# Optimization experiments

Measured on AMD Instinct MI355X. Metric: run time of the kernel, lower is better.

Reference implementation:

```python
import jax, jax.numpy as jnp
import numpy as np

B, N, C, H = 4, 1024, 1024, 16
D = C // H  # head_dim = 64
SCALE = D ** -0.5


def setup_inputs() -> dict:
    key = jax.random.key(0)
    ks = jax.random.split(key, 7)
    std = 0.02
    return {
        "xq": jax.random.normal(ks[0], (B, N, C), dtype=jnp.float32),
        "xk": jax.random.normal(ks[1], (B, N, C), dtype=jnp.float32),
        "xv": jax.random.normal(ks[2], (B, N, C), dtype=jnp.float32),
        # torch nn.Linear weights are [out_features, in_features]
        "Wq": jax.random.normal(ks[3], (C, C), dtype=jnp.float32) * std,
        "Wkv": jax.random.normal(ks[4], (2 * C, C), dtype=jnp.float32) * std,
        "Wp": jax.random.normal(ks[5], (C, C), dtype=jnp.float32) * std,
        "bp": jax.random.normal(ks[6], (C,), dtype=jnp.float32) * std,
    }


def reference(xq, xk, xv, Wq, Wkv, Wp, bp):
    b, nq, c = xq.shape
    nk = xk.shape[1]
    # q projection -> [B, H, Nq, D]
    q = (xq @ Wq.T).reshape(b, nq, H, D).transpose(0, 2, 1, 3)
    # HPA: shared projection produces K and V from xk (xv unused)
    kv = xk @ Wkv.T  # [B, Nk, 2C]
    k, v = jnp.split(kv, 2, axis=-1)
    k = k.reshape(b, nk, H, D).transpose(0, 2, 1, 3)  # [B, H, Nk, D]
    v = v.reshape(b, nk, H, D).transpose(0, 2, 1, 3)  # [B, H, Nk, D]
    # pre-softmax scores (attn_save in original)
    attn = jnp.einsum("bhqd,bhkd->bhqk", q, k) * SCALE  # [B, H, Nq, Nk]
    p = jax.nn.softmax(attn, axis=-1)
    x = jnp.einsum("bhqk,bhkd->bhqd", p, v)  # [B, H, Nq, D]
    x = x.transpose(0, 2, 1, 3).reshape(b, nq, c)
    x = x @ Wp.T + bp
    # returns (x transposed to [Nq, B, C], mean-over-heads pre-softmax scores)
    return x.transpose(1, 0, 2), attn.sum(axis=1) / H
```

## Files before the change

kernel.cpp:

```cpp
#include <hip/hip_runtime.h>
#include <hip/hip_bf16.h>
#include <stdint.h>

typedef __attribute__((ext_vector_type(8))) short bf16x8;
typedef __attribute__((ext_vector_type(4))) short bf16x4;
typedef __attribute__((ext_vector_type(4))) float f32x4;

#define B_DIM 4
#define N_DIM 1024
#define C_DIM 1024
#define NT 16

#define QSCALE 0.18033688011112042f
#define OUT1_ALPHA 0.04332169878499658f

__device__ __forceinline__ ushort f2bf(float f) {
  union { float f; uint32_t u; } v; v.f = f;
  uint32_t r = (v.u + 0x7FFFu + ((v.u >> 16) & 1u)) >> 16;
  return (ushort)r;
}

__device__ __forceinline__ uint32_t cvtpk(float lo, float hi) {
  uint32_t r;
  asm("v_cvt_pk_bf16_f32 %0, %1, %2" : "=v"(r) : "v"(lo), "v"(hi));
  return r;
}

__device__ __forceinline__ void gload_lds16(const void* g, void* l) {
  __builtin_amdgcn_global_load_lds(
      (const __attribute__((address_space(1))) void*)g,
      (__attribute__((address_space(3))) void*)l, 16, 0, 0);
}

__device__ __forceinline__ f32x4 mfma16(bf16x8 a, bf16x8 b, f32x4 c) {
  return __builtin_amdgcn_mfma_f32_16x16x32_bf16(a, b, c, 0, 0, 0);
}

__device__ __forceinline__ void mfma16x16(bf16x4 a, bf16x4 b, f32x4& c) {
  asm("v_mfma_f32_16x16x16_bf16 %0, %1, %2, %0" : "+v"(c) : "v"(a), "v"(b));
}

template <int N>
__device__ __forceinline__ void waitcnt_vm() {
  asm volatile("s_waitcnt vmcnt(%0)" ::"i"(N) : "memory");
}

__global__ __launch_bounds__(256) void cvt_all(
    const float* __restrict__ xq, const float* __restrict__ xk,
    const float* __restrict__ Wq, const float* __restrict__ Wkv,
    const float* __restrict__ Wp, ushort* __restrict__ xq_b,
    ushort* __restrict__ xk_b, ushort* __restrict__ Wq_b,
    ushort* __restrict__ Wkv_b, ushort* __restrict__ Wp_b) {
  int bid = blockIdx.x;
  const float* s;
  ushort* d;
  int off;
  if (bid < 4096) { s = xq; d = xq_b; off = bid; }
  else if (bid < 8192) { s = xk; d = xk_b; off = bid - 4096; }
  else if (bid < 9216) { s = Wq; d = Wq_b; off = bid - 8192; }
  else if (bid < 11264) { s = Wkv; d = Wkv_b; off = bid - 9216; }
  else { s = Wp; d = Wp_b; off = bid - 11264; }
  int i = off * 1024 + threadIdx.x * 4;
  float4 v = *(const float4*)(s + i);
  ushort4 o;
  o.x = f2bf(v.x); o.y = f2bf(v.y); o.z = f2bf(v.z); o.w = f2bf(v.w);
  *(ushort4*)(d + i) = o;
}

template <int MODE, int BN>
__device__ __forceinline__ void gemm_core(
    ushort* As, ushort* Bs, const ushort* A, const ushort* Bm, float* Cf,
    ushort* Cb, int K, int lda, int ldb, int ldc, int m0, int n0, float alpha,
    const float* bias) {
  constexpr int MR = (BN == 128) ? 4 : 2;
  constexpr int WM = (BN == 128) ? 64 : 32;
  constexpr int ABUF = 4096, BBUF = BN * 32;
  constexpr int NLD = (BN == 128) ? 4 : 3;
  const int tid = threadIdx.x;
  const int l = tid & 63, wv = tid >> 6, lg = l >> 4, lr = l & 15;
  const int wr = (BN == 128) ? (wv >> 1) : wv;
  const int wc = (BN == 128) ? (wv & 1) : 0;
  const int r0 = tid >> 2;
  const int cs = ((tid & 3) ^ ((r0 >> 1) & 3)) * 8;
  const int wb = (tid & ~63) * 8;
  const int cA = ((lg ^ ((lr >> 1) & 3)) << 3);
  const ushort* Ar0 = A + (size_t)(m0 + r0) * lda + cs;
  const ushort* Ar1 = A + (size_t)(m0 + 64 + r0) * lda + cs;
  const ushort* Br0 = Bm + (size_t)(n0 + r0) * ldb + cs;
  const ushort* Br1 = Bm + (size_t)(n0 + 64 + r0) * ldb + cs;

#define STAGE(t, bi)                                                     \
  {                                                                      \
    const int k0_ = (t) << 5;                                            \
    gload_lds16(Ar0 + k0_, As + (bi) * ABUF + wb);                       \
    gload_lds16(Ar1 + k0_, As + (bi) * ABUF + 2048 + wb);                \
    gload_lds16(Br0 + k0_, Bs + (bi) * BBUF + wb);                       \
    if (BN == 128) gload_lds16(Br1 + k0_, Bs + (bi) * BBUF + 2048 + wb); \
  }

  const int nk = K >> 5;
  STAGE(0, 0);
  STAGE(1, 1);
  f32x4 acc[MR][4] = {};
  waitcnt_vm<NLD>();
  __builtin_amdgcn_sched_barrier(0);
  __builtin_amdgcn_s_barrier();
  __builtin_amdgcn_sched_barrier(0);
  int b0 = 0;
  for (int t = 0; t < nk; ++t) {
    const int b2 = (b0 + 2 >= 3) ? b0 - 1 : b0 + 2;
    if (t + 2 < nk) STAGE(t + 2, b2);
    const ushort* Ab = As + b0 * ABUF;
    const ushort* Bb = Bs + b0 * BBUF;
    bf16x8 af[MR], bfr[4];
#pragma unroll
    for (int m = 0; m < MR; m++)
      af[m] = *(const bf16x8*)&Ab[(wr * WM + m * 16 + lr) * 32 + cA];
#pragma unroll
    for (int n = 0; n < 4; n++)
      bfr[n] = *(const bf16x8*)&Bb[(wc * 64 + n * 16 + lr) * 32 + cA];
    __builtin_amdgcn_s_setprio(1);
#pragma unroll
    for (int m = 0; m < MR; m++)
#pragma unroll
      for (int n = 0; n < 4; n++)
        acc[m][n] = mfma16(af[m], bfr[n], acc[m][n]);
    __builtin_amdgcn_s_setprio(0);
    if (t + 1 < nk) {
      if (t + 2 < nk) waitcnt_vm<NLD>(); else waitcnt_vm<0>();
      __builtin_amdgcn_sched_barrier(0);
      __builtin_amdgcn_s_barrier();
      __builtin_amdgcn_sched_barrier(0);
    }
    b0 = (b0 + 1 >= 3) ? 0 : b0 + 1;
  }
#undef STAGE

#pragma unroll
  for (int m = 0; m < MR; m++) {
    const int row = m0 + wr * WM + m * 16 + lg * 4;
#pragma unroll
    for (int n = 0; n < 4; n++) {
      const int col = n0 + wc * 64 + n * 16 + lr;
#pragma unroll
      for (int r = 0; r < 4; r++) {
        float v = acc[m][n][r];
        if (MODE == 0) {
          Cb[(size_t)(row + r) * ldc + col] = f2bf(v * alpha);
        } else if (MODE == 1) {
          Cf[(size_t)(row + r) * ldc + col] = v * alpha;
        } else {
          int gm = row + r;
          int bb = gm >> 10, nq = gm & 1023;
          Cf[((size_t)nq * B_DIM + bb) * C_DIM + col] = v + bias[col];
        }
      }
    }
  }
}

template <int MODE, int BN>
__global__ __launch_bounds__(256) void gemm_bt(
    const ushort* __restrict__ A, const ushort* __restrict__ Bm,
    float* __restrict__ Cf, ushort* __restrict__ Cb, int K, int lda, int ldb,
    int ldc, long sA, long sB, long sC, float alpha,
    const float* __restrict__ bias) {
  __shared__ ushort As[3 * 4096];
  __shared__ ushort Bs[3 * BN * 32];
  const int z = blockIdx.z;
  float* cf = (MODE == 0) ? nullptr : (Cf + (size_t)z * sC);
  ushort* cb = (MODE == 0) ? (Cb + (size_t)z * sC) : nullptr;
  gemm_core<MODE, BN>(As, Bs, A + (size_t)z * sA, Bm + (size_t)z * sB, cf, cb,
                      K, lda, ldb, ldc, blockIdx.y * 128, blockIdx.x * BN,
                      alpha, bias);
}

__global__ __launch_bounds__(256) void gemm_dual(
    const ushort* __restrict__ A0, const ushort* __restrict__ B0,
    ushort* __restrict__ C0, const ushort* __restrict__ A1,
    const ushort* __restrict__ B1, ushort* __restrict__ C1) {
  __shared__ ushort As[3 * 4096];
  __shared__ ushort Bs[3 * 4096];
  int bid = blockIdx.x;
  if (bid < 256) {
    gemm_core<0, 128>(As, Bs, A0, B0, nullptr, C0, 1024, 1024, 1024, 1024,
                      (bid >> 3) * 128, (bid & 7) * 128, QSCALE, nullptr);
  } else {
    bid -= 256;
    gemm_core<0, 128>(As, Bs, A1, B1, nullptr, C1, 1024, 1024, 1024, 2048,
                      (bid >> 4) * 128, (bid & 15) * 128, 1.f, nullptr);
  }
}

__global__ __launch_bounds__(256) void flash_out1(
    const ushort* __restrict__ Qp, const ushort* __restrict__ KVp,
    ushort* __restrict__ O, float* __restrict__ out1) {
  __shared__ ushort sm[20480];
  int bid = blockIdx.x;

  if (bid >= 1024) {
    int b2 = bid - 1024;
    int z = b2 >> 7;
    gemm_core<1, 64>(sm, sm + 12288, Qp + (size_t)z * 1048576,
                     KVp + (size_t)z * 2097152, out1 + (size_t)z * 1048576,
                     nullptr, 1024, 1024, 2048, 1024, ((b2 >> 4) & 7) * 128,
                     (b2 & 15) * 64, OUT1_ALPHA, nullptr);
    return;
  }

  ushort* Ks0 = sm;
  ushort* Vs0 = sm + 8192;
  ushort* Qs = sm + 16384;

  const int tid = threadIdx.x;
  const int w = tid >> 6, l = tid & 63;
  const int lg = l >> 4, lr = l & 15;
  const int bh = bid >> 4;
  const int b = bh >> 4, h = bh & 15;
  const int q0 = (bid & 15) * 64;

  const ushort* Qg =
      Qp + (size_t)b * (N_DIM * C_DIM) + (size_t)q0 * C_DIM + h * 64;
  const ushort* Kg = KVp + (size_t)b * (N_DIM * 2 * C_DIM) + h * 64;
  const ushort* Vg = Kg + C_DIM;

  const int sr = tid >> 3;
  const int sc = (tid & 7) ^ (sr & 7);
  const int wb = (tid & ~63) * 8;
  const int vrow = (l & 31) >> 1;
  const int vdc = ((l >> 5) << 4) + (l & 1) * 8;

#define STAGE_K(kt2, buf)                                                   \
  {                                                                         \
    gload_lds16(Kg + (size_t)((kt2) + sr) * 2048 + sc * 8, (buf) + wb);     \
    gload_lds16(Kg + (size_t)((kt2) + 32 + sr) * 2048 + sc * 8,             \
                (buf) + 2048 + wb);                                         \
  }
#define STAGE_V(kt2, buf)                                                   \
  {                                                                         \
    gload_lds16(Vg + (size_t)((kt2) + w * 16 + vrow) * 2048 + vdc,          \
                (buf) + (w * 4 + 0) * 256);                                 \
    gload_lds16(Vg + (size_t)((kt2) + w * 16 + vrow) * 2048 + 32 + vdc,     \
                (buf) + (w * 4 + 2) * 256);                                 \
  }

  gload_lds16(Qg + (size_t)sr * C_DIM + sc * 8, Qs + wb);
  gload_lds16(Qg + (size_t)(32 + sr) * C_DIM + sc * 8, Qs + 2048 + wb);
  STAGE_K(0, Ks0);
  STAGE_V(0, Vs0);
  __syncthreads();
  const int qrow = w * 16 + lr;
  bf16x8 qa0 = *(const bf16x8*)&Qs[qrow * 64 + ((lg ^ (qrow & 7)) << 3)];
  bf16x8 qa1 = *(const bf16x8*)&Qs[qrow * 64 + (((lg + 4) ^ (qrow & 7)) << 3)];

  f32x4 oacc[4] = {};
  float lp = 0.f;
  const uint32_t vbase =
      (uint32_t)(uintptr_t)(__attribute__((address_space(3))) ushort*)Vs0 +
      (uint32_t)(l * 8);

  for (int t = 0; t < NT; ++t) {
    const int cur = t & 1;
    ushort* Kc = Ks0 + cur * 4096;
    if (t + 1 < NT) {
      const int kt2 = (t + 1) * 64;
      STAGE_K(kt2, Ks0 + (cur ^ 1) * 4096);
      STAGE_V(kt2, Vs0 + (cur ^ 1) * 4096);
    }

    f32x4 s[4];
    __builtin_amdgcn_s_setprio(1);
#pragma unroll
    for (int kf = 0; kf < 4; kf++) {
      const int krow = kf * 16 + lr;
      bf16x8 kb0 = *(const bf16x8*)&Kc[krow * 64 + ((lg ^ (krow & 7)) << 3)];
      bf16x8 kb1 =
          *(const bf16x8*)&Kc[krow * 64 + (((lg + 4) ^ (krow & 7)) << 3)];
      f32x4 zz = {};
      zz = mfma16(kb0, qa0, zz);
      zz = mfma16(kb1, qa1, zz);
      s[kf] = zz;
    }
    __builtin_amdgcn_s_setprio(0);

    bf16x4 pa[4];
#pragma unroll
    for (int kf = 0; kf < 4; kf++) {
      float p0 = exp2f(s[kf][0]), p1 = exp2f(s[kf][1]);
      float p2 = exp2f(s[kf][2]), p3 = exp2f(s[kf][3]);
      lp += (p0 + p1) + (p2 + p3);
      union { uint32_t u[2]; bf16x4 v; } pk;
      pk.u[0] = cvtpk(p0, p1);
      pk.u[1] = cvtpk(p2, p3);
      pa[kf] = pk.v;
    }

    const uint32_t trb = vbase + cur * 8192;
    __builtin_amdgcn_s_setprio(1);
#define PV_DF(df, O0, O1, O2, O3)                                          \
  {                                                                        \
    bf16x4 v0, v1, v2, v3;                                                 \
    asm volatile("ds_read_b64_tr_b16 %0, %1 offset:" #O0                   \
                 : "=v"(v0) : "v"(trb));                                   \
    asm volatile("ds_read_b64_tr_b16 %0, %1 offset:" #O1                   \
                 : "=v"(v1) : "v"(trb));                                   \
    asm volatile("ds_read_b64_tr_b16 %0, %1 offset:" #O2                   \
                 : "=v"(v2) : "v"(trb));                                   \
    asm volatile("ds_read_b64_tr_b16 %0, %1 offset:" #O3                   \
                 : "=v"(v3) : "v"(trb));                                   \
    asm volatile("s_waitcnt lgkmcnt(0)" ::: "memory");                     \
    __builtin_amdgcn_sched_barrier(0);                                     \
    mfma16x16(pa[0], v0, oacc[df]);                                        \
    mfma16x16(pa[1], v1, oacc[df]);                                        \
    mfma16x16(pa[2], v2, oacc[df]);                                        \
    mfma16x16(pa[3], v3, oacc[df]);                                        \
  }
    PV_DF(0, 0, 2048, 4096, 6144)
    PV_DF(1, 512, 2560, 4608, 6656)
    PV_DF(2, 1024, 3072, 5120, 7168)
    PV_DF(3, 1536, 3584, 5632, 7680)
#undef PV_DF
    __builtin_amdgcn_s_setprio(0);

    __syncthreads();
  }
#undef STAGE_K
#undef STAGE_V

  lp += __shfl_xor(lp, 16);
  lp += __shfl_xor(lp, 32);
  float linv[4];
#pragma unroll
  for (int r = 0; r < 4; r++) linv[r] = 1.0f / __shfl(lp, lg * 4 + r);

  ushort* Og = O + (size_t)b * (N_DIM * C_DIM) +
               (size_t)(q0 + w * 16 + lg * 4) * C_DIM + h * 64;
#pragma unroll
  for (int df = 0; df < 4; df++)
#pragma unroll
    for (int r = 0; r < 4; r++)
      Og[(size_t)r * C_DIM + df * 16 + lr] = f2bf(oacc[df][r] * linv[r]);
}

extern "C" void kernel_launch(void* const* d_in, const int* in_sizes, int n_in,
                              void* d_out, int out_size, void* d_ws,
                              size_t ws_size, hipStream_t stream) {
  const float* xq = (const float*)d_in[0];
  const float* xk = (const float*)d_in[1];
  const float* Wq = (const float*)d_in[3];
  const float* Wkv = (const float*)d_in[4];
  const float* Wp = (const float*)d_in[5];
  const float* bp = (const float*)d_in[6];

  ushort* ws = (ushort*)d_ws;
  ushort* xq_b = ws;
  ushort* xk_b = xq_b + 4194304;
  ushort* Wq_b = xk_b + 4194304;
  ushort* Wkv_b = Wq_b + 1048576;
  ushort* Wp_b = Wkv_b + 2097152;
  ushort* Qp = Wp_b + 1048576;
  ushort* KVp = Qp + 4194304;
  ushort* Ob = KVp + 8388608;

  float* out0 = (float*)d_out;
  float* out1 = out0 + 4194304;

  cvt_all<<<12288, 256, 0, stream>>>(xq, xk, Wq, Wkv, Wp, xq_b, xk_b, Wq_b,
                                     Wkv_b, Wp_b);
  gemm_dual<<<768, 256, 0, stream>>>(xq_b, Wq_b, Qp, xk_b, Wkv_b, KVp);
  flash_out1<<<1536, 256, 0, stream>>>(Qp, KVp, Ob, out1);
  gemm_bt<2, 64><<<dim3(16, 32, 1), 256, 0, stream>>>(
      Ob, Wp_b, out0, nullptr, 1024, 1024, 1024, 1024, 0, 0, 0, 1.f, bp);
}
```

Baseline: 213.8 us.

## Replace 256-thread GEMMs with single-wave 64x64 tile GEMM kernels

Swaps the 4-wave 128x128 (and 128x64) tiled GEMMs for Q/KV projection and the output projection with a new single-wave kernel. Each block computes a 64x64 tile, loads directly into LDS and double-buffers it with a 2-stage prefetch. This gives many more, smaller blocks and avoids cross-wave synchronisation. In exchange each tile reuses less data, so global/L2 traffic per FLOP goes up.

```diff
diff --git a/kernel.cpp b/kernel.cpp
--- a/kernel.cpp
+++ b/kernel.cpp
@@ -65,6 +65,109 @@
   ushort4 o;
   o.x = f2bf(v.x); o.y = f2bf(v.y); o.z = f2bf(v.z); o.w = f2bf(v.w);
   *(ushort4*)(d + i) = o;
+}
+
+template <int MODE>
+__device__ __forceinline__ void gemm_nb_core(
+    ushort* Ls, const ushort* A, const ushort* Bm, int lda, int ldb,
+    float* Cf, ushort* Cb, int ldc, int crow0, int ccol0, float alpha,
+    const float* bias) {
+  const int l = threadIdx.x & 63;
+  const int lg = l >> 4, lr = l & 15;
+  const int cs = ((l & 3) ^ ((l >> 3) & 3)) * 8;
+  const ushort* Ar = A + (size_t)(l >> 2) * lda + cs;
+  const ushort* Br = Bm + (size_t)(l >> 2) * ldb + cs;
+  ushort* LA = Ls;
+  ushort* LB = Ls + 4096;
+  const int cA = (lg ^ ((lr >> 1) & 3)) << 3;
+
+#define NBSTAGE(t, bi)                                          \
+  {                                                             \
+    const int k0_ = (t) << 5;                                   \
+    gload_lds16(Ar + k0_, LA + (bi) * 2048);                    \
+    gload_lds16(Ar + (size_t)16 * lda + k0_, LA + (bi) * 2048 + 512);  \
+    gload_lds16(Ar + (size_t)32 * lda + k0_, LA + (bi) * 2048 + 1024); \
+    gload_lds16(Ar + (size_t)48 * lda + k0_, LA + (bi) * 2048 + 1536); \
+    gload_lds16(Br + k0_, LB + (bi) * 2048);                    \
+    gload_lds16(Br + (size_t)16 * ldb + k0_, LB + (bi) * 2048 + 512);  \
+    gload_lds16(Br + (size_t)32 * ldb + k0_, LB + (bi) * 2048 + 1024); \
+    gload_lds16(Br + (size_t)48 * ldb + k0_, LB + (bi) * 2048 + 1536); \
+  }
+
+  f32x4 acc[4][4] = {};
+  NBSTAGE(0, 0);
+  NBSTAGE(1, 1);
+  for (int t = 0; t < 32; ++t) {
+    if (t + 1 < 32) waitcnt_vm<8>(); else waitcnt_vm<0>();
+    const int bo = (t & 1) * 2048;
+    bf16x8 af[4], bf[4];
+#pragma unroll
+    for (int m = 0; m < 4; m++)
+      af[m] = *(const bf16x8*)&LA[bo + (m * 16 + lr) * 32 + cA];
+#pragma unroll
+    for (int n = 0; n < 4; n++)
+      bf[n] = *(const bf16x8*)&LB[bo + (n * 16 + lr) * 32 + cA];
+    __builtin_amdgcn_s_setprio(1);
+#pragma unroll
+    for (int m = 0; m < 4; m++)
+#pragma unroll
+      for (int n = 0; n < 4; n++)
+        acc[m][n] = mfma16(af[m], bf[n], acc[m][n]);
+    __builtin_amdgcn_s_setprio(0);
+    if (t + 2 < 32) NBSTAGE(t + 2, t & 1);
+  }
+#undef NBSTAGE
+
+#pragma unroll
+  for (int m = 0; m < 4; m++) {
+    const int row = crow0 + m * 16 + lg * 4;
+#pragma unroll
+    for (int n = 0; n < 4; n++) {
+      const int col = ccol0 + n * 16 + lr;
+#pragma unroll
+      for (int r = 0; r < 4; r++) {
+        float v = acc[m][n][r];
+        if (MODE == 0) {
+          Cb[(size_t)(row + r) * ldc + col] = f2bf(v * alpha);
+        } else {
+          int gm = row + r;
+          int bb = gm >> 10, nq = gm & 1023;
+          Cf[((size_t)nq * B_DIM + bb) * C_DIM + col] = v + bias[col];
+        }
+      }
+    }
+  }
+}
+
+__global__ __launch_bounds__(64) void gemm_nb_dual(
+    const ushort* __restrict__ xq_b, const ushort* __restrict__ xk_b,
+    const ushort* __restrict__ Wq_b, const ushort* __restrict__ Wkv_b,
+    ushort* __restrict__ Qp, ushort* __restrict__ KVp) {
+  __shared__ ushort Ls[8192];
+  int bid = blockIdx.x;
+  if (bid < 1024) {
+    int mt = bid >> 4, nt = bid & 15;
+    gemm_nb_core<0>(Ls, xq_b + (size_t)mt * 64 * 1024,
+                    Wq_b + (size_t)nt * 64 * 1024, 1024, 1024, nullptr, Qp,
+                    1024, mt * 64, nt * 64, QSCALE, nullptr);
+  } else {
+    int b2 = bid - 1024;
+    int mt = b2 >> 5, nt = b2 & 31;
+    gemm_nb_core<0>(Ls, xk_b + (size_t)mt * 64 * 1024,
+                    Wkv_b + (size_t)nt * 64 * 1024, 1024, 1024, nullptr, KVp,
+                    2048, mt * 64, nt * 64, 1.f, nullptr);
+  }
+}
+
+__global__ __launch_bounds__(64) void gemm_nb_proj(
+    const ushort* __restrict__ Ob, const ushort* __restrict__ Wp_b,
+    float* __restrict__ out0, const float* __restrict__ bias) {
+  __shared__ ushort Ls[8192];
+  int bid = blockIdx.x;
+  int mt = bid >> 4, nt = bid & 15;
+  gemm_nb_core<2>(Ls, Ob + (size_t)mt * 64 * 1024,
+                  Wp_b + (size_t)nt * 64 * 1024, 1024, 1024, out0, nullptr,
+                  1024, mt * 64, nt * 64, 1.f, bias);
 }
 
 template <int MODE, int BN>
@@ -159,39 +262,6 @@
   }
 }
 
-template <int MODE, int BN>
-__global__ __launch_bounds__(256) void gemm_bt(
-    const ushort* __restrict__ A, const ushort* __restrict__ Bm,
-    float* __restrict__ Cf, ushort* __restrict__ Cb, int K, int lda, int ldb,
-    int ldc, long sA, long sB, long sC, float alpha,
-    const float* __restrict__ bias) {
-  __shared__ ushort As[3 * 4096];
-  __shared__ ushort Bs[3 * BN * 32];
-  const int z = blockIdx.z;
-  float* cf = (MODE == 0) ? nullptr : (Cf + (size_t)z * sC);
-  ushort* cb = (MODE == 0) ? (Cb + (size_t)z * sC) : nullptr;
-  gemm_core<MODE, BN>(As, Bs, A + (size_t)z * sA, Bm + (size_t)z * sB, cf, cb,
-                      K, lda, ldb, ldc, blockIdx.y * 128, blockIdx.x * BN,
-                      alpha, bias);
-}
-
-__global__ __launch_bounds__(256) void gemm_dual(
-    const ushort* __restrict__ A0, const ushort* __restrict__ B0,
-    ushort* __restrict__ C0, const ushort* __restrict__ A1,
-    const ushort* __restrict__ B1, ushort* __restrict__ C1) {
-  __shared__ ushort As[3 * 4096];
-  __shared__ ushort Bs[3 * 4096];
-  int bid = blockIdx.x;
-  if (bid < 256) {
-    gemm_core<0, 128>(As, Bs, A0, B0, nullptr, C0, 1024, 1024, 1024, 1024,
-                      (bid >> 3) * 128, (bid & 7) * 128, QSCALE, nullptr);
-  } else {
-    bid -= 256;
-    gemm_core<0, 128>(As, Bs, A1, B1, nullptr, C1, 1024, 1024, 1024, 2048,
-                      (bid >> 4) * 128, (bid & 15) * 128, 1.f, nullptr);
-  }
-}
-
 __global__ __launch_bounds__(256) void flash_out1(
     const ushort* __restrict__ Qp, const ushort* __restrict__ KVp,
     ushort* __restrict__ O, float* __restrict__ out1) {
@@ -367,8 +437,7 @@
 
   cvt_all<<<12288, 256, 0, stream>>>(xq, xk, Wq, Wkv, Wp, xq_b, xk_b, Wq_b,
                                      Wkv_b, Wp_b);
-  gemm_dual<<<768, 256, 0, stream>>>(xq_b, Wq_b, Qp, xk_b, Wkv_b, KVp);
+  gemm_nb_dual<<<3072, 64, 0, stream>>>(xq_b, xk_b, Wq_b, Wkv_b, Qp, KVp);
   flash_out1<<<1536, 256, 0, stream>>>(Qp, KVp, Ob, out1);
-  gemm_bt<2, 64><<<dim3(16, 32, 1), 256, 0, stream>>>(
-      Ob, Wp_b, out0, nullptr, 1024, 1024, 1024, 1024, 0, 0, 0, 1.f, bp);
-}
+  gemm_nb_proj<<<1024, 64, 0, stream>>>(Ob, Wp_b, out0, bp);
+}
```

Measured after the change: 228.2 us. 6.7% more time.

## Shrink flash kernel LDS, load Q directly, remap dual-GEMM block order

Applied to the files above, without the earlier changes.

The flash/out1 fused kernel's shared memory drops from 40KB to 32KB. The score GEMM branch now uses a new double-buffered, unswizzled gemm2_core instead of the triple-buffered core, and Q fragments are read straight from global memory instead of being staged through LDS. The dual projection GEMM remaps block IDs so that consecutive blocks spread across the two sub-GEMMs, which is likely meant to balance work across XCDs. The aim is higher occupancy and less LDS traffic, at the risk of LDS bank conflicts from the unswizzled layout and less latency hiding with two buffers instead of three. Batched-stride parameters are also removed from gemm_bt.

```diff
diff --git a/kernel.cpp b/kernel.cpp
--- a/kernel.cpp
+++ b/kernel.cpp
@@ -163,16 +163,11 @@
 __global__ __launch_bounds__(256) void gemm_bt(
     const ushort* __restrict__ A, const ushort* __restrict__ Bm,
     float* __restrict__ Cf, ushort* __restrict__ Cb, int K, int lda, int ldb,
-    int ldc, long sA, long sB, long sC, float alpha,
-    const float* __restrict__ bias) {
+    int ldc, float alpha, const float* __restrict__ bias) {
   __shared__ ushort As[3 * 4096];
   __shared__ ushort Bs[3 * BN * 32];
-  const int z = blockIdx.z;
-  float* cf = (MODE == 0) ? nullptr : (Cf + (size_t)z * sC);
-  ushort* cb = (MODE == 0) ? (Cb + (size_t)z * sC) : nullptr;
-  gemm_core<MODE, BN>(As, Bs, A + (size_t)z * sA, Bm + (size_t)z * sB, cf, cb,
-                      K, lda, ldb, ldc, blockIdx.y * 128, blockIdx.x * BN,
-                      alpha, bias);
+  gemm_core<MODE, BN>(As, Bs, A, Bm, Cf, Cb, K, lda, ldb, ldc,
+                      blockIdx.y * 128, blockIdx.x * BN, alpha, bias);
 }
 
 __global__ __launch_bounds__(256) void gemm_dual(
@@ -181,7 +176,7 @@
     const ushort* __restrict__ B1, ushort* __restrict__ C1) {
   __shared__ ushort As[3 * 4096];
   __shared__ ushort Bs[3 * 4096];
-  int bid = blockIdx.x;
+  int bid = (blockIdx.x & 7) * 96 + (blockIdx.x >> 3);
   if (bid < 256) {
     gemm_core<0, 128>(As, Bs, A0, B0, nullptr, C0, 1024, 1024, 1024, 1024,
                       (bid >> 3) * 128, (bid & 7) * 128, QSCALE, nullptr);
@@ -192,25 +187,94 @@
   }
 }
 
+template <int MODE, int BN>
+__device__ __forceinline__ void gemm2_core(
+    ushort* As, ushort* Bs, const ushort* A, const ushort* Bm, float* Cf,
+    ushort* Cb, int K, int lda, int ldb, int ldc, int m0, int n0, float alpha,
+    const float* bias) {
+  constexpr int MR = (BN == 128) ? 4 : 2;
+  constexpr int WM = (BN == 128) ? 64 : 32;
+  constexpr int BBUF = BN * 32;
+  const int tid = threadIdx.x;
+  const int l = tid & 63, wv = tid >> 6, lg = l >> 4, lr = l & 15;
+  const int wr = (BN == 128) ? (wv >> 1) : wv;
+  const int wc = (BN == 128) ? (wv & 1) : 0;
+  const int r0 = tid >> 2, c0 = (tid & 3) * 8;
+  const int wb = (tid & ~63) * 8;
+  const ushort* Arow0 = A + (size_t)(m0 + r0) * lda + c0;
+  const ushort* Arow1 = A + (size_t)(m0 + 64 + r0) * lda + c0;
+  const ushort* Brow0 = Bm + (size_t)(n0 + r0) * ldb + c0;
+  const ushort* Brow1 =
+      (BN == 128) ? (Bm + (size_t)(n0 + 64 + r0) * ldb + c0) : Brow0;
+
+  gload_lds16(Arow0, As + wb);
+  gload_lds16(Arow1, As + 2048 + wb);
+  gload_lds16(Brow0, Bs + wb);
+  if (BN == 128) gload_lds16(Brow1, Bs + 2048 + wb);
+  f32x4 acc[MR][4] = {};
+  __syncthreads();
+  const int nk = K >> 5;
+  for (int t = 0; t < nk; ++t) {
+    const int pA = (t & 1) ? 4096 : 0;
+    const int pB = (t & 1) ? BBUF : 0;
+    if (t + 1 < nk) {
+      const int nA = pA ^ 4096, nB = pB ^ BBUF;
+      const int k0 = (t + 1) << 5;
+      gload_lds16(Arow0 + k0, As + nA + wb);
+      gload_lds16(Arow1 + k0, As + nA + 2048 + wb);
+      gload_lds16(Brow0 + k0, Bs + nB + wb);
+      if (BN == 128) gload_lds16(Brow1 + k0, Bs + nB + 2048 + wb);
+    }
+    bf16x8 af[MR], bfr[4];
+#pragma unroll
+    for (int m = 0; m < MR; m++)
+      af[m] = *(const bf16x8*)&As[pA + (wr * WM + m * 16 + lr) * 32 + lg * 8];
+#pragma unroll
+    for (int n = 0; n < 4; n++)
+      bfr[n] = *(const bf16x8*)&Bs[pB + (wc * 64 + n * 16 + lr) * 32 + lg * 8];
+#pragma unroll
+    for (int m = 0; m < MR; m++)
+#pragma unroll
+      for (int n = 0; n < 4; n++)
+        acc[m][n] = mfma16(af[m], bfr[n], acc[m][n]);
+    __syncthreads();
+  }
+
+#pragma unroll
+  for (int m = 0; m < MR; m++) {
+    const int row = m0 + wr * WM + m * 16 + lg * 4;
+#pragma unroll
+    for (int n = 0; n < 4; n++) {
+      const int col = n0 + wc * 64 + n * 16 + lr;
+#pragma unroll
+      for (int r = 0; r < 4; r++) {
+        float v = acc[m][n][r];
+        if (MODE == 1) {
+          Cf[(size_t)(row + r) * ldc + col] = v * alpha;
+        }
+      }
+    }
+  }
+}
+
 __global__ __launch_bounds__(256) void flash_out1(
     const ushort* __restrict__ Qp, const ushort* __restrict__ KVp,
     ushort* __restrict__ O, float* __restrict__ out1) {
-  __shared__ ushort sm[20480];
+  __shared__ ushort sm[16384];
   int bid = blockIdx.x;
 
   if (bid >= 1024) {
     int b2 = bid - 1024;
     int z = b2 >> 7;
-    gemm_core<1, 64>(sm, sm + 12288, Qp + (size_t)z * 1048576,
-                     KVp + (size_t)z * 2097152, out1 + (size_t)z * 1048576,
-                     nullptr, 1024, 1024, 2048, 1024, ((b2 >> 4) & 7) * 128,
-                     (b2 & 15) * 64, OUT1_ALPHA, nullptr);
+    gemm2_core<1, 64>(sm, sm + 8192, Qp + (size_t)z * 1048576,
+                      KVp + (size_t)z * 2097152, out1 + (size_t)z * 1048576,
+                      nullptr, 1024, 1024, 2048, 1024, ((b2 >> 4) & 7) * 128,
+                      (b2 & 15) * 64, OUT1_ALPHA, nullptr);
     return;
   }
 
   ushort* Ks0 = sm;
   ushort* Vs0 = sm + 8192;
-  ushort* Qs = sm + 16384;
 
   const int tid = threadIdx.x;
   const int w = tid >> 6, l = tid & 63;
@@ -244,14 +308,12 @@
                 (buf) + (w * 4 + 2) * 256);                                 \
   }
 
-  gload_lds16(Qg + (size_t)sr * C_DIM + sc * 8, Qs + wb);
-  gload_lds16(Qg + (size_t)(32 + sr) * C_DIM + sc * 8, Qs + 2048 + wb);
   STAGE_K(0, Ks0);
   STAGE_V(0, Vs0);
+  const int qrow = w * 16 + lr;
+  bf16x8 qa0 = *(const bf16x8*)(Qg + (size_t)qrow * C_DIM + lg * 8);
+  bf16x8 qa1 = *(const bf16x8*)(Qg + (size_t)qrow * C_DIM + 32 + lg * 8);
   __syncthreads();
-  const int qrow = w * 16 + lr;
-  bf16x8 qa0 = *(const bf16x8*)&Qs[qrow * 64 + ((lg ^ (qrow & 7)) << 3)];
-  bf16x8 qa1 = *(const bf16x8*)&Qs[qrow * 64 + (((lg + 4) ^ (qrow & 7)) << 3)];
 
   f32x4 oacc[4] = {};
   float lp = 0.f;
@@ -370,5 +432,5 @@
   gemm_dual<<<768, 256, 0, stream>>>(xq_b, Wq_b, Qp, xk_b, Wkv_b, KVp);
   flash_out1<<<1536, 256, 0, stream>>>(Qp, KVp, Ob, out1);
   gemm_bt<2, 64><<<dim3(16, 32, 1), 256, 0, stream>>>(
-      Ob, Wp_b, out0, nullptr, 1024, 1024, 1024, 1024, 0, 0, 0, 1.f, bp);
-}
+      Ob, Wp_b, out0, nullptr, 1024, 1024, 1024, 1024, 1.f, bp);
+}
```

Result: no change. 215.2 us (+0.6%).
